# Kernel optimization log

Measured on AMD Instinct MI355X. Metric: run time of the kernel, lower is better.

Reference implementation:

```python
import jax, jax.numpy as jnp
import numpy as np

N_ATOM = 16384
N_EDGE = 262144
D_IN = 32
D_OUT = 32
N_CHEB = 3
N_CH = 8
CUTOFF = 5.0
GAMMA = 4.0

_SI = ['ec,co->eo', 'eci,co->eoi', 'ecij,co->eoij']


def _self_interact(d, W):
    # per-way channel mixing (SelfInteractionLayer): linear over channel axis, no bias
    return {w: jnp.einsum(_SI[w], d[w], W[w]) for w in d}


def _tensor_product(x, y, max_z):
    # TensorProductLayer: for each (x_way a, y_way b) couple into every allowed
    # z_way (|a-b| <= z <= a+b, a+b+z even) by contracting k=(a+b-z)/2 spatial axes.
    z = {}
    for a, xa in x.items():
        for b, yb in y.items():
            for zw in range(abs(a - b), min(a + b, max_z) + 1, 2):
                k = (a + b - zw) // 2
                E, C = xa.shape[:2]
                out = jnp.einsum('ecik,ecjk->ecij',
                                 xa.reshape(E, C, 3 ** (a - k), 3 ** k),
                                 yb.reshape(E, C, 3 ** (b - k), 3 ** k))
                out = out.reshape((E, C) + (3,) * zw)
                z[zw] = z.get(zw, 0.0) + out
    return z


def setup_inputs() -> dict:
    key = jax.random.key(0)
    ks = jax.random.split(key, 13)
    return {
        'node0': jax.random.normal(ks[0], (N_ATOM, D_IN), dtype=jnp.float32),
        'node1': jax.random.normal(ks[1], (N_ATOM, D_IN, 3), dtype=jnp.float32),
        'node2': jax.random.normal(ks[2], (N_ATOM, D_IN, 3, 3), dtype=jnp.float32),
        'coord': jax.random.normal(ks[3], (N_ATOM, 3), dtype=jnp.float32) * 3.0,
        'spin': jax.random.normal(ks[4], (N_ATOM, 3), dtype=jnp.float32),
        'idx_i': jax.random.randint(ks[5], (N_EDGE,), 0, N_ATOM),
        'idx_j': jax.random.randint(ks[6], (N_EDGE,), 0, N_ATOM),
        'rbf_w': jax.random.normal(ks[7], (3, N_CH, D_OUT * N_CHEB), dtype=jnp.float32) * 0.2,
        'rbf_b': jax.random.normal(ks[8], (3, D_OUT * N_CHEB), dtype=jnp.float32) * 0.1,
        'srbf_w': jax.random.normal(ks[9], (3, N_CH, D_OUT * N_CHEB), dtype=jnp.float32) * 0.2,
        'srbf_b': jax.random.normal(ks[10], (3, D_OUT * N_CHEB), dtype=jnp.float32) * 0.1,
        'U_w': jax.random.normal(ks[11], (3, D_IN, D_OUT), dtype=jnp.float32) / np.sqrt(D_IN),
        'V_w': jax.random.normal(ks[12], (3, N_CHEB * D_OUT, D_OUT), dtype=jnp.float32) / np.sqrt(N_CHEB * D_OUT),
    }


def reference(node0, node1, node2, coord, spin, idx_i, idx_j,
              rbf_w, rbf_b, srbf_w, srbf_b, U_w, V_w):
    E = idx_i.shape[0]
    # find_distances: edge vectors / distances / unit vectors
    rij = coord[idx_j] - coord[idx_i]                      # [E,3]
    dij = jnp.sqrt(jnp.sum(rij * rij, -1) + 1e-12)         # [E]
    uij = rij / dij[:, None]
    # radial_fn(dij): Gaussian basis with cosine cutoff -> [E, N_CH]
    centers = jnp.linspace(0.0, CUTOFF, N_CH)
    fc = 0.5 * (jnp.cos(jnp.pi * jnp.clip(dij / CUTOFF, 0.0, 1.0)) + 1.0)
    rbf = jnp.exp(-GAMMA * (dij[:, None] - centers) ** 2) * fc[:, None]
    # find_spin: mi = |spin|, si = unit spin, sij = cos angle between edge spins
    mi = jnp.sqrt(jnp.sum(spin * spin, -1) + 1e-12)        # [N]
    si = spin / mi[:, None]
    sij = jnp.sum(si[idx_i] * si[idx_j], -1)               # [E], in [-1,1]
    scent = jnp.linspace(0.0, 3.0, N_CH)
    srbf = jnp.exp(-GAMMA * (mi[:, None] - scent) ** 2)    # [N, N_CH]
    # ChebyshevPoly(n_max=3) on sij: T0, T1, T2
    cheb = jnp.stack([jnp.ones_like(sij), sij, 2.0 * sij * sij - 1.0], -1)  # [E,3]
    # gather neighbour features and apply U
    node = {0: node0[idx_j], 1: node1[idx_j], 2: node2[idx_j]}
    node = _self_interact(node, U_w)
    # moments of the unit vector
    moments = {0: jnp.ones((E,), dtype=uij.dtype), 1: uij,
               2: uij[:, :, None] * uij[:, None, :]}
    r = {}
    for way in range(3):
        sb = srbf @ srbf_w[way] + srbf_b[way]              # [N, 3*D_OUT]
        hehe = (rbf @ rbf_w[way] + rbf_b[way]) * sb[idx_i] * sb[idx_j]  # [E, 3*D_OUT]
        xixi = (hehe.reshape(E, N_CHEB, D_OUT) * cheb[:, :, None]).reshape(E, -1)
        mom = moments[way].reshape((E, 1) + (3,) * way)
        r[way] = mom * xixi.reshape((E, -1) + (1,) * way)  # [E, 3*D_OUT, 3^way]
    r = _self_interact(r, V_w)
    z = _tensor_product(node, r, 2)
    return (z[0], z[1], z[2])
```

## Files before the change

kernel.cpp:

```cpp
#include <hip/hip_runtime.h>
#include <math.h>

#define NA 16384
#define NE 262144

#define SI_OFF   0
#define SB_OFF   (NA*3)
#define NM_OFF   (SB_OFF + 3*NA*96)
#define RWT_OFF  (NM_OFF + NA*512)
#define WS_FLOATS (RWT_OFF + 3*96*8)
#define HIST_OFF (WS_FLOATS)
#define PERM_OFF (HIST_OFF + NA)

__global__ __launch_bounds__(256) void repack_rw_k(const float* __restrict__ rbf_w,
                                                   float* __restrict__ ws) {
    int t = blockIdx.x * 256 + threadIdx.x;
    if (t >= 2304) return;
    int k = t & 7;
    int c = (t >> 3) % 96;
    int w = t / 768;
    ws[RWT_OFF + t] = rbf_w[w * 768 + k * 96 + c];
}

__global__ __launch_bounds__(256) void hist_zero_k(int* __restrict__ hist) {
    int t = blockIdx.x * 256 + threadIdx.x;
    if (t < NA) hist[t] = 0;
}

__global__ __launch_bounds__(256) void hist_k(const int* __restrict__ idx_j,
                                              int* __restrict__ hist) {
    int e = blockIdx.x * 256 + threadIdx.x;
    if (e < NE) atomicAdd(&hist[idx_j[e]], 1);
}

__global__ __launch_bounds__(256) void scan_k(int* __restrict__ hist) {
    __shared__ int sums[256];
    int t = threadIdx.x;
    int lo = t * 64;
    int s = 0;
    for (int k = 0; k < 64; ++k) s += hist[lo + k];
    sums[t] = s;
    __syncthreads();
    for (int off = 1; off < 256; off <<= 1) {
        int v = (t >= off) ? sums[t - off] : 0;
        __syncthreads();
        sums[t] += v;
        __syncthreads();
    }
    int ex = sums[t] - s;
    for (int k = 0; k < 64; ++k) {
        int c = hist[lo + k];
        hist[lo + k] = ex;
        ex += c;
    }
}

__global__ __launch_bounds__(256) void scatter_k(const int* __restrict__ idx_j,
                                                 int* __restrict__ hist,
                                                 int* __restrict__ perm) {
    int e = blockIdx.x * 256 + threadIdx.x;
    if (e < NE) {
        int pos = atomicAdd(&hist[idx_j[e]], 1);
        perm[pos] = e;
    }
}

__global__ __launch_bounds__(256) void atom_prep_k(
    const float* __restrict__ node0, const float* __restrict__ node1,
    const float* __restrict__ node2, const float* __restrict__ spin,
    const float* __restrict__ srbf_w, const float* __restrict__ srbf_b,
    const float* __restrict__ U_w, float* __restrict__ ws)
{
    const int wave = threadIdx.x >> 6;
    const int lane = threadIdx.x & 63;
    const int a = blockIdx.x * 4 + wave;
    if (a >= NA) return;

    float sx = spin[a*3+0], sy = spin[a*3+1], sz = spin[a*3+2];
    float mi = sqrtf(sx*sx + sy*sy + sz*sz + 1e-12f);
    float inv = 1.0f / mi;
    if (lane < 3) ws[SI_OFF + a*3 + lane] = spin[a*3 + lane] * inv;

    float srbf[8];
    #pragma unroll
    for (int k = 0; k < 8; ++k) {
        float d = mi - (float)k * (3.0f / 7.0f);
        srbf[k] = expf(-4.0f * d * d);
    }

    #pragma unroll
    for (int w = 0; w < 3; ++w) {
        #pragma unroll
        for (int rep = 0; rep < 2; ++rep) {
            int c = rep * 64 + lane;
            if (c < 96) {
                float acc = srbf_b[w*96 + c];
                #pragma unroll
                for (int k = 0; k < 8; ++k)
                    acc = fmaf(srbf[k], srbf_w[w*768 + k*96 + c], acc);
                ws[SB_OFF + ((size_t)w*NA + a)*96 + c] = acc;
            }
        }
    }

    const int o = lane & 31;
    const int h = lane >> 5;
    float acc[13];
    #pragma unroll
    for (int sp = 0; sp < 13; ++sp) acc[sp] = 0.0f;

    for (int cc = 0; cc < 16; ++cc) {
        int c = h * 16 + cc;
        float f0 = node0[a*32 + c];
        float u0 = U_w[0*1024 + c*32 + o];
        float u1 = U_w[1*1024 + c*32 + o];
        float u2 = U_w[2*1024 + c*32 + o];
        acc[0] = fmaf(f0, u0, acc[0]);
        #pragma unroll
        for (int jj = 0; jj < 3; ++jj)
            acc[1+jj] = fmaf(node1[a*96 + c*3 + jj], u1, acc[1+jj]);
        #pragma unroll
        for (int ij = 0; ij < 9; ++ij)
            acc[4+ij] = fmaf(node2[a*288 + c*9 + ij], u2, acc[4+ij]);
    }
    #pragma unroll
    for (int sp = 0; sp < 13; ++sp)
        acc[sp] += __shfl_xor(acc[sp], 32);

    if (h == 0) {
        float* p = ws + NM_OFF + (size_t)a*512 + o*16;
        *(float4*)(p + 0)  = make_float4(acc[0], acc[1], acc[2], acc[3]);
        *(float4*)(p + 4)  = make_float4(acc[4], acc[5], acc[6], acc[7]);
        *(float4*)(p + 8)  = make_float4(acc[8], acc[9], acc[10], acc[11]);
        *(float4*)(p + 12) = make_float4(acc[12], 0.f, 0.f, 0.f);
    }
}

__global__ __launch_bounds__(256) void edge_s_k(
    const float* __restrict__ coord, const int* __restrict__ idx_i,
    const int* __restrict__ idx_j, const float* __restrict__ rbf_b,
    const float* __restrict__ V_w, const float* __restrict__ ws,
    const int* __restrict__ perm, float* __restrict__ out)
{
    const int t = blockIdx.x * 256 + threadIdx.x;
    const int e = perm[t];
    const int i = idx_i[e];
    const int j = idx_j[e];

    float rx = coord[j*3+0] - coord[i*3+0];
    float ry = coord[j*3+1] - coord[i*3+1];
    float rz = coord[j*3+2] - coord[i*3+2];
    float d2 = rx*rx + ry*ry + rz*rz + 1e-12f;
    float dij = sqrtf(d2);
    float invd = 1.0f / dij;
    float ux = rx*invd, uy = ry*invd, uz = rz*invd;

    float tt = fminf(dij * 0.2f, 1.0f);
    float fc = 0.5f * (cosf(3.14159265358979323846f * tt) + 1.0f);
    float rbf[8];
    #pragma unroll
    for (int k = 0; k < 8; ++k) {
        float d = dij - (float)k * (5.0f / 7.0f);
        rbf[k] = expf(-4.0f * d * d) * fc;
    }

    const float* si = ws + SI_OFF;
    float sij = si[i*3+0]*si[j*3+0] + si[i*3+1]*si[j*3+1] + si[i*3+2]*si[j*3+2];
    float cheb1 = sij;
    float cheb2 = 2.0f * sij * sij - 1.0f;

    float* o2 = out + (size_t)NE*128 + (size_t)e*288;

    #pragma unroll 1
    for (int w = 0; w < 3; ++w) {
        const float* sbi = ws + SB_OFF + ((size_t)w*NA + i)*96;
        const float* sbj = ws + SB_OFF + ((size_t)w*NA + j)*96;
        const float* rwt = ws + RWT_OFF + w*768;
        const float* rbb = rbf_b + w*96;
        const float* vw  = V_w + w*3072;

        float s[32];
        #pragma unroll
        for (int o = 0; o < 32; ++o) s[o] = 0.0f;

        #pragma unroll
        for (int tb = 0; tb < 3; ++tb) {
            float chb = (tb == 0) ? 1.0f : ((tb == 1) ? cheb1 : cheb2);
            #pragma unroll 4
            for (int cc = 0; cc < 8; ++cc) {
                int c0 = tb*32 + cc*4;
                float4 vi = *(const float4*)(sbi + c0);
                float4 vj = *(const float4*)(sbj + c0);
                float pv[4];
                pv[0] = vi.x * vj.x; pv[1] = vi.y * vj.y;
                pv[2] = vi.z * vj.z; pv[3] = vi.w * vj.w;
                #pragma unroll
                for (int q = 0; q < 4; ++q) {
                    int c = c0 + q;
                    float rm = rbb[c];
                    #pragma unroll
                    for (int k = 0; k < 8; ++k)
                        rm = fmaf(rbf[k], rwt[c*8 + k], rm);
                    float g = rm * pv[q] * chb;
                    const float* vc = vw + c*32;
                    #pragma unroll
                    for (int o = 0; o < 32; ++o)
                        s[o] = fmaf(vc[o], g, s[o]);
                }
            }
        }

        #pragma unroll
        for (int og = 0; og < 8; ++og)
            *(float4*)(o2 + w*32 + og*4) =
                make_float4(s[og*4+0], s[og*4+1], s[og*4+2], s[og*4+3]);
    }

    *(float4*)(o2 + 96)  = make_float4(ux, uy, uz, 0.0f);
    #pragma unroll
    for (int k = 1; k < 8; ++k)
        *(float4*)(o2 + 96 + k*4) = make_float4(0.f, 0.f, 0.f, 0.f);
}

__device__ __forceinline__ void edge_epilogue(
    int e, int q,
    float4 v0, float4 v1, float4 v2, float4 uu,
    const float4* nmv, const float* nd4, float* __restrict__ out)
{
    float ux = uu.x, uy = uu.y, uz = uu.z;
    float c0[4] = {v0.x, v0.y, v0.z, v0.w};
    float c1[4] = {v1.x, v1.y, v1.z, v1.w};
    float c2[4] = {v2.x, v2.y, v2.z, v2.w};

    float r0[4], r1[12], r2[36];
    #pragma unroll
    for (int oo = 0; oo < 4; ++oo) {
        float4 va  = nmv[oo*3+0];
        float4 vb  = nmv[oo*3+1];
        float4 vc4 = nmv[oo*3+2];
        float nd   = nd4[oo];
        float n0 = va.x, n1x = va.y, n1y = va.z, n1z = va.w;
        float t00 = vb.x, t01 = vb.y, t02 = vb.z, t10 = vb.w;
        float t11 = vc4.x, t12 = vc4.y, t20 = vc4.z, t21 = vc4.w, t22 = nd;
        float s0 = c0[oo], s1 = c1[oo], s2 = c2[oo];

        float d1 = n1x*ux + n1y*uy + n1z*uz;
        float m0 = t00*ux + t01*uy + t02*uz;
        float m1 = t10*ux + t11*uy + t12*uz;
        float m2 = t20*ux + t21*uy + t22*uz;
        float qq = m0*ux + m1*uy + m2*uz;

        r0[oo] = n0*s0 + d1*s1 + qq*s2;

        float w1 = n0*s1 + s2*d1;
        r1[oo*3+0] = w1*ux + n1x*s0 + s1*m0;
        r1[oo*3+1] = w1*uy + n1y*s0 + s1*m1;
        r1[oo*3+2] = w1*uz + n1z*s0 + s1*m2;

        float n0s2 = n0*s2;
        float a0 = ux*n0s2 + s1*n1x + s2*m0;
        float a1 = uy*n0s2 + s1*n1y + s2*m1;
        float a2 = uz*n0s2 + s1*n1z + s2*m2;
        r2[oo*9+0] = a0*ux + s0*t00;
        r2[oo*9+1] = a0*uy + s0*t01;
        r2[oo*9+2] = a0*uz + s0*t02;
        r2[oo*9+3] = a1*ux + s0*t10;
        r2[oo*9+4] = a1*uy + s0*t11;
        r2[oo*9+5] = a1*uz + s0*t12;
        r2[oo*9+6] = a2*ux + s0*t20;
        r2[oo*9+7] = a2*uy + s0*t21;
        r2[oo*9+8] = a2*uz + s0*t22;
    }

    *(float4*)(out + (size_t)e*32 + q*4) =
        make_float4(r0[0], r0[1], r0[2], r0[3]);

    float* p1 = out + (size_t)NE*32 + (size_t)e*96 + q*12;
    #pragma unroll
    for (int k = 0; k < 3; ++k)
        *(float4*)(p1 + k*4) =
            make_float4(r1[k*4+0], r1[k*4+1], r1[k*4+2], r1[k*4+3]);

    float* p2 = out + (size_t)NE*128 + (size_t)e*288 + q*36;
    #pragma unroll
    for (int k = 0; k < 9; ++k)
        *(float4*)(p2 + k*4) =
            make_float4(r2[k*4+0], r2[k*4+1], r2[k*4+2], r2[k*4+3]);
}

__global__ __launch_bounds__(256, 2) void edge_out_k(
    const int* __restrict__ idx_j, const float* __restrict__ ws,
    float* __restrict__ out)
{
    const int t = blockIdx.x * 256 + threadIdx.x;
    const int g = t >> 3;
    const int q = t & 7;
    const int ea = g;
    const int eb = g + NE/2;
    const int ja = idx_j[ea];
    const int jb = idx_j[eb];

    const float* o2a = out + (size_t)NE*128 + (size_t)ea*288;
    const float* o2b = out + (size_t)NE*128 + (size_t)eb*288;
    const float* nma = ws + NM_OFF + (size_t)ja*512 + q*64;
    const float* nmb = ws + NM_OFF + (size_t)jb*512 + q*64;

    float4 a_v0 = *(const float4*)(o2a + q*4);
    float4 a_v1 = *(const float4*)(o2a + 32 + q*4);
    float4 a_v2 = *(const float4*)(o2a + 64 + q*4);
    float4 a_uu = *(const float4*)(o2a + 96);
    float4 a_nm[12];
    float  a_nd[4];
    #pragma unroll
    for (int oo = 0; oo < 4; ++oo) {
        a_nm[oo*3+0] = *(const float4*)(nma + oo*16 + 0);
        a_nm[oo*3+1] = *(const float4*)(nma + oo*16 + 4);
        a_nm[oo*3+2] = *(const float4*)(nma + oo*16 + 8);
        a_nd[oo]     = nma[oo*16 + 12];
    }
    float4 b_v0 = *(const float4*)(o2b + q*4);
    float4 b_v1 = *(const float4*)(o2b + 32 + q*4);
    float4 b_v2 = *(const float4*)(o2b + 64 + q*4);
    float4 b_uu = *(const float4*)(o2b + 96);
    float4 b_nm[12];
    float  b_nd[4];
    #pragma unroll
    for (int oo = 0; oo < 4; ++oo) {
        b_nm[oo*3+0] = *(const float4*)(nmb + oo*16 + 0);
        b_nm[oo*3+1] = *(const float4*)(nmb + oo*16 + 4);
        b_nm[oo*3+2] = *(const float4*)(nmb + oo*16 + 8);
        b_nd[oo]     = nmb[oo*16 + 12];
    }
    __builtin_amdgcn_sched_barrier(0);

    edge_epilogue(ea, q, a_v0, a_v1, a_v2, a_uu, a_nm, a_nd, out);
    edge_epilogue(eb, q, b_v0, b_v1, b_v2, b_uu, b_nm, b_nd, out);
}

extern "C" void kernel_launch(void* const* d_in, const int* in_sizes, int n_in,
                              void* d_out, int out_size, void* d_ws, size_t ws_size,
                              hipStream_t stream) {
    const float* node0  = (const float*)d_in[0];
    const float* node1  = (const float*)d_in[1];
    const float* node2  = (const float*)d_in[2];
    const float* coord  = (const float*)d_in[3];
    const float* spin   = (const float*)d_in[4];
    const int*   idx_i  = (const int*)d_in[5];
    const int*   idx_j  = (const int*)d_in[6];
    const float* rbf_w  = (const float*)d_in[7];
    const float* rbf_b  = (const float*)d_in[8];
    const float* srbf_w = (const float*)d_in[9];
    const float* srbf_b = (const float*)d_in[10];
    const float* U_w    = (const float*)d_in[11];
    const float* V_w    = (const float*)d_in[12];
    float* out = (float*)d_out;
    float* ws  = (float*)d_ws;
    int*   wsi = (int*)d_ws;
    int*   hist = wsi + HIST_OFF;
    int*   perm = wsi + PERM_OFF;

    repack_rw_k<<<(2304 + 255) / 256, 256, 0, stream>>>(rbf_w, ws);
    atom_prep_k<<<NA / 4, 256, 0, stream>>>(node0, node1, node2, spin,
                                            srbf_w, srbf_b, U_w, ws);
    hist_zero_k<<<NA / 256, 256, 0, stream>>>(hist);
    hist_k<<<NE / 256, 256, 0, stream>>>(idx_j, hist);
    scan_k<<<1, 256, 0, stream>>>(hist);
    scatter_k<<<NE / 256, 256, 0, stream>>>(idx_j, hist, perm);
    edge_s_k<<<NE / 256, 256, 0, stream>>>(coord, idx_i, idx_j, rbf_b,
                                           V_w, ws, perm, out);
    edge_out_k<<<(NE / 2 * 8) / 256, 256, 0, stream>>>(idx_j, ws, out);
}
```

Before: 496.3 us.

## Repack per-atom workspace into atom-major SB and component-major node tables

```diff
diff --git a/kernel.cpp b/kernel.cpp
--- a/kernel.cpp
+++ b/kernel.cpp
@@ -7,7 +7,7 @@
 #define SI_OFF   0
 #define SB_OFF   (NA*3)
 #define NM_OFF   (SB_OFF + 3*NA*96)
-#define RWT_OFF  (NM_OFF + NA*512)
+#define RWT_OFF  (NM_OFF + NA*416)
 #define WS_FLOATS (RWT_OFF + 3*96*8)
 #define HIST_OFF (WS_FLOATS)
 #define PERM_OFF (HIST_OFF + NA)
@@ -98,7 +98,7 @@
                 #pragma unroll
                 for (int k = 0; k < 8; ++k)
                     acc = fmaf(srbf[k], srbf_w[w*768 + k*96 + c], acc);
-                ws[SB_OFF + ((size_t)w*NA + a)*96 + c] = acc;
+                ws[SB_OFF + (size_t)a*288 + w*96 + c] = acc;
             }
         }
     }
@@ -128,11 +128,10 @@
         acc[sp] += __shfl_xor(acc[sp], 32);
 
     if (h == 0) {
-        float* p = ws + NM_OFF + (size_t)a*512 + o*16;
-        *(float4*)(p + 0)  = make_float4(acc[0], acc[1], acc[2], acc[3]);
-        *(float4*)(p + 4)  = make_float4(acc[4], acc[5], acc[6], acc[7]);
-        *(float4*)(p + 8)  = make_float4(acc[8], acc[9], acc[10], acc[11]);
-        *(float4*)(p + 12) = make_float4(acc[12], 0.f, 0.f, 0.f);
+        float* p = ws + NM_OFF + (size_t)a*416;
+        #pragma unroll
+        for (int sp = 0; sp < 13; ++sp)
+            p[sp*32 + o] = acc[sp];
     }
 }
 
@@ -170,11 +169,13 @@
     float cheb2 = 2.0f * sij * sij - 1.0f;
 
     float* o2 = out + (size_t)NE*128 + (size_t)e*288;
+    const float* sbi_a = ws + SB_OFF + (size_t)i*288;
+    const float* sbj_a = ws + SB_OFF + (size_t)j*288;
 
     #pragma unroll 1
     for (int w = 0; w < 3; ++w) {
-        const float* sbi = ws + SB_OFF + ((size_t)w*NA + i)*96;
-        const float* sbj = ws + SB_OFF + ((size_t)w*NA + j)*96;
+        const float* sbi = sbi_a + w*96;
+        const float* sbj = sbj_a + w*96;
         const float* rwt = ws + RWT_OFF + w*768;
         const float* rbb = rbf_b + w*96;
         const float* vw  = V_w + w*3072;
@@ -222,10 +223,19 @@
         *(float4*)(o2 + 96 + k*4) = make_float4(0.f, 0.f, 0.f, 0.f);
 }
 
+__device__ __forceinline__ float get4(const float4& v, int oo) {
+    switch (oo) {
+        case 0:  return v.x;
+        case 1:  return v.y;
+        case 2:  return v.z;
+        default: return v.w;
+    }
+}
+
 __device__ __forceinline__ void edge_epilogue(
     int e, int q,
     float4 v0, float4 v1, float4 v2, float4 uu,
-    const float4* nmv, const float* nd4, float* __restrict__ out)
+    const float4* cm, float* __restrict__ out)
 {
     float ux = uu.x, uy = uu.y, uz = uu.z;
     float c0[4] = {v0.x, v0.y, v0.z, v0.w};
@@ -235,13 +245,11 @@
     float r0[4], r1[12], r2[36];
     #pragma unroll
     for (int oo = 0; oo < 4; ++oo) {
-        float4 va  = nmv[oo*3+0];
-        float4 vb  = nmv[oo*3+1];
-        float4 vc4 = nmv[oo*3+2];
-        float nd   = nd4[oo];
-        float n0 = va.x, n1x = va.y, n1y = va.z, n1z = va.w;
-        float t00 = vb.x, t01 = vb.y, t02 = vb.z, t10 = vb.w;
-        float t11 = vc4.x, t12 = vc4.y, t20 = vc4.z, t21 = vc4.w, t22 = nd;
+        float n0  = get4(cm[0], oo);
+        float n1x = get4(cm[1], oo), n1y = get4(cm[2], oo), n1z = get4(cm[3], oo);
+        float t00 = get4(cm[4], oo), t01 = get4(cm[5], oo), t02 = get4(cm[6], oo);
+        float t10 = get4(cm[7], oo), t11 = get4(cm[8], oo), t12 = get4(cm[9], oo);
+        float t20 = get4(cm[10], oo), t21 = get4(cm[11], oo), t22 = get4(cm[12], oo);
         float s0 = c0[oo], s1 = c1[oo], s2 = c2[oo];
 
         float d1 = n1x*ux + n1y*uy + n1z*uz;
@@ -302,39 +310,31 @@
 
     const float* o2a = out + (size_t)NE*128 + (size_t)ea*288;
     const float* o2b = out + (size_t)NE*128 + (size_t)eb*288;
-    const float* nma = ws + NM_OFF + (size_t)ja*512 + q*64;
-    const float* nmb = ws + NM_OFF + (size_t)jb*512 + q*64;
+    const float* nma = ws + NM_OFF + (size_t)ja*416;
+    const float* nmb = ws + NM_OFF + (size_t)jb*416;
 
     float4 a_v0 = *(const float4*)(o2a + q*4);
     float4 a_v1 = *(const float4*)(o2a + 32 + q*4);
     float4 a_v2 = *(const float4*)(o2a + 64 + q*4);
     float4 a_uu = *(const float4*)(o2a + 96);
-    float4 a_nm[12];
-    float  a_nd[4];
-    #pragma unroll
-    for (int oo = 0; oo < 4; ++oo) {
-        a_nm[oo*3+0] = *(const float4*)(nma + oo*16 + 0);
-        a_nm[oo*3+1] = *(const float4*)(nma + oo*16 + 4);
-        a_nm[oo*3+2] = *(const float4*)(nma + oo*16 + 8);
-        a_nd[oo]     = nma[oo*16 + 12];
-    }
+    float4 a_cm[13];
+    #pragma unroll
+    for (int k = 0; k < 13; ++k)
+        a_cm[k] = *(const float4*)(nma + k*32 + q*4);
+
     float4 b_v0 = *(const float4*)(o2b + q*4);
     float4 b_v1 = *(const float4*)(o2b + 32 + q*4);
     float4 b_v2 = *(const float4*)(o2b + 64 + q*4);
     float4 b_uu = *(const float4*)(o2b + 96);
-    float4 b_nm[12];
-    float  b_nd[4];
-    #pragma unroll
-    for (int oo = 0; oo < 4; ++oo) {
-        b_nm[oo*3+0] = *(const float4*)(nmb + oo*16 + 0);
-        b_nm[oo*3+1] = *(const float4*)(nmb + oo*16 + 4);
-        b_nm[oo*3+2] = *(const float4*)(nmb + oo*16 + 8);
-        b_nd[oo]     = nmb[oo*16 + 12];
-    }
+    float4 b_cm[13];
+    #pragma unroll
+    for (int k = 0; k < 13; ++k)
+        b_cm[k] = *(const float4*)(nmb + k*32 + q*4);
+
     __builtin_amdgcn_sched_barrier(0);
 
-    edge_epilogue(ea, q, a_v0, a_v1, a_v2, a_uu, a_nm, a_nd, out);
-    edge_epilogue(eb, q, b_v0, b_v1, b_v2, b_uu, b_nm, b_nd, out);
+    edge_epilogue(ea, q, a_v0, a_v1, a_v2, a_uu, a_cm, out);
+    edge_epilogue(eb, q, b_v0, b_v1, b_v2, b_uu, b_cm, out);
 }
 
 extern "C" void kernel_launch(void* const* d_in, const int* in_sizes, int n_in,
```

Measured after the change: 508.5 us. 2.4% more time.
